# Optimization experiments

Measured on AMD Instinct MI355X. Metric: run time of the kernel, lower is better.

The kernel has to match this reference:

```python
import jax, jax.numpy as jnp
import numpy as np

N = 100000   # nodes
E = 1600000  # edges
F_IN = 64
HID = 64
N_HLIN = 64
N_PRED = 1
G = 128      # graphs in batch


def setup_inputs() -> dict:
    key = jax.random.key(0)
    ks = jax.random.split(key, 12)
    x = jax.random.normal(ks[0], (N, F_IN), dtype=jnp.float32)
    edge_index = jax.random.randint(ks[1], (2, E), 0, N, dtype=jnp.int64)
    batch = jnp.sort(jax.random.randint(ks[2], (N,), 0, G, dtype=jnp.int64))
    def glorot(k, fan_in, fan_out):
        return jax.random.normal(k, (fan_in, fan_out), dtype=jnp.float32) / np.float32(np.sqrt(fan_in))
    return {
        "x": x, "edge_index": edge_index, "batch": batch,
        "W1": glorot(ks[3], F_IN, HID), "b1": jnp.zeros((HID,), jnp.float32),
        "W2": glorot(ks[4], HID, HID),  "b2": jnp.zeros((HID,), jnp.float32),
        "W3": glorot(ks[5], HID, HID),  "b3": jnp.zeros((HID,), jnp.float32),
        "W4": glorot(ks[6], HID, N_HLIN), "b4": jnp.zeros((N_HLIN,), jnp.float32),
        "lin_w": glorot(ks[7], N_HLIN, N_PRED),
        "lin_b": jnp.zeros((N_PRED,), jnp.float32),
    }


def reference(x, edge_index, batch, W1, b1, W2, b2, W3, b3, W4, b4, lin_w, lin_b):
    # GCNConv semantics (PyG default): add self-loops, symmetric deg^-1/2 normalization,
    # h' = scatter_add(norm * (h W)[src] -> dst) + b
    loop = jnp.arange(N, dtype=edge_index.dtype)
    src = jnp.concatenate([edge_index[0], loop])  # [E+N]
    dst = jnp.concatenate([edge_index[1], loop])  # [E+N]
    deg = jax.ops.segment_sum(jnp.ones_like(dst, dtype=x.dtype), dst, num_segments=N)
    dis = deg ** -0.5  # deg >= 1 thanks to self-loops
    norm = (dis[src] * dis[dst])[:, None]  # [E+N, 1]

    def gcn_conv(h, W, b):
        h = h @ W                      # [N, out]
        msg = h[src] * norm            # edge gather + scale
        agg = jax.ops.segment_sum(msg, dst, num_segments=N)  # scatter-add
        return agg + b

    h = jax.nn.relu(gcn_conv(x, W1, b1))
    h = jax.nn.relu(gcn_conv(h, W2, b2))
    h = jax.nn.relu(gcn_conv(h, W3, b3))
    h = gcn_conv(h, W4, b4)

    # global_mean_pool over graph ids
    sums = jax.ops.segment_sum(h, batch, num_segments=G)          # [G, N_HLIN]
    cnts = jax.ops.segment_sum(jnp.ones((N,), h.dtype), batch, num_segments=G)
    pooled = sums / jnp.maximum(cnts, 1.0)[:, None]
    # dropout is identity in eval mode
    return pooled @ lin_w + lin_b  # [G, N_PRED]
```

## Files before the change

### kernel.cpp

```cpp
#include <hip/hip_runtime.h>
#include <type_traits>

#define NN 100000
#define NE 1600000
#define FD 64
#define NG 128
#define NB ((NN + 255) >> 8)
#define CAP 6144
#define SRCMASK 0x1FFFF
#define ZR NN

typedef _Float16 f16x8 __attribute__((ext_vector_type(8)));
typedef _Float16 f16x4 __attribute__((ext_vector_type(4)));
typedef float f32x4 __attribute__((ext_vector_type(4)));

__global__ void bhist_k(const int* __restrict__ dst, int* __restrict__ bhist) {
    __shared__ int h[NB];
    int t = threadIdx.x;
    for (int i = t; i < NB; i += 256) h[i] = 0;
    __syncthreads();
    int base = blockIdx.x * 4096;
#pragma unroll
    for (int i = 0; i < 16; i++) {
        int e = base + i * 256 + t;
        if (e < NE) atomicAdd(&h[dst[e] >> 8], 1);
    }
    __syncthreads();
    for (int i = t; i < NB; i += 256)
        if (h[i]) atomicAdd(&bhist[i], h[i]);
}

__global__ void bscan_k(const int* __restrict__ bhist, int* __restrict__ bbase,
                        int* __restrict__ gcursor, _Float16* __restrict__ zrow) {
    __shared__ int sS[512];
    int t = threadIdx.x;
    if (t < 8) ((int4*)zrow)[t] = make_int4(0, 0, 0, 0);
    sS[t] = (t < NB) ? bhist[t] : 0;
    __syncthreads();
    for (int off = 1; off < 512; off <<= 1) {
        int x = (t >= off) ? sS[t - off] : 0;
        __syncthreads();
        if (t >= off) sS[t] += x;
        __syncthreads();
    }
    int excl = (t == 0) ? 0 : sS[t - 1];
    if (t < NB) { bbase[t] = excl; gcursor[t] = excl; }
    if (t == NB) bbase[NB] = NE;
}

__global__ void part1_k(const int* __restrict__ src, const int* __restrict__ dst,
                        int* __restrict__ gcursor, int* __restrict__ part) {
    __shared__ int hist[NB];
    __shared__ int resv[NB];
    __shared__ int lcur[NB];
    int t = threadIdx.x;
    for (int i = t; i < NB; i += 256) { hist[i] = 0; lcur[i] = 0; }
    __syncthreads();
    int base = blockIdx.x * 4096;
    int s[16], d[16];
#pragma unroll
    for (int i = 0; i < 16; i++) {
        int e = base + i * 256 + t;
        if (e < NE) {
            s[i] = src[e]; d[i] = dst[e];
            atomicAdd(&hist[d[i] >> 8], 1);
        } else d[i] = -1;
    }
    __syncthreads();
    for (int b = t; b < NB; b += 256)
        if (hist[b]) resv[b] = atomicAdd(&gcursor[b], hist[b]);
    __syncthreads();
#pragma unroll
    for (int i = 0; i < 16; i++) {
        if (d[i] >= 0) {
            int b = d[i] >> 8;
            int off = atomicAdd(&lcur[b], 1);
            part[resv[b] + off] = s[i] | ((d[i] & 255) << 17);
        }
    }
}

__global__ void csr2_k(const int* __restrict__ part, const int* __restrict__ bbase,
                       int* __restrict__ rowptr, float* __restrict__ dis,
                       int* __restrict__ entries) {
    __shared__ int sA[CAP];
    __shared__ int sB[CAP];
    __shared__ int cntL[256];
    __shared__ int posL[256];
    __shared__ int locL[256];
    int b = blockIdx.x, t = threadIdx.x;
    int n0 = b << 8;
    int nCnt = min(256, NN - n0);
    cntL[t] = 0; posL[t] = 0;
    __syncthreads();
    int e0 = bbase[b], e1 = bbase[b + 1];
    int cnt = e1 - e0;

    for (int i = t; i < cnt; i += 256) {
        int pk = part[e0 + i];
        if (i < CAP) sA[i] = pk;
        atomicAdd(&cntL[(pk >> 17) & 255], 1);
    }
    __syncthreads();

    locL[t] = cntL[t];
    __syncthreads();
    for (int off = 1; off < 256; off <<= 1) {
        int x = (t >= off) ? locL[t - off] : 0;
        __syncthreads();
        if (t >= off) locL[t] += x;
        __syncthreads();
    }
    int excl = (t == 0) ? 0 : locL[t - 1];
    __syncthreads();
    locL[t] = excl;
    __syncthreads();

    if (t < nCnt) {
        rowptr[n0 + t] = e0 + locL[t];
        dis[n0 + t] = rsqrtf((float)cntL[t] + 1.0f);
    }
    if (b == NB - 1 && t == 0) rowptr[NN] = NE;

    for (int i = t; i < cnt; i += 256) {
        int pk = (i < CAP) ? sA[i] : part[e0 + i];
        int ln = (pk >> 17) & 255;
        int sv = pk & SRCMASK;
        int pos = atomicAdd(&posL[ln], 1);
        int idx = locL[ln] + pos;
        if (idx < CAP) sB[idx] = sv;
        else entries[e0 + idx] = sv;
    }
    __syncthreads();
    int lim = min(cnt, CAP);
    for (int i = t; i < lim; i += 256)
        entries[e0 + i] = sB[i];
}

template <typename TIN>
__global__ __launch_bounds__(256) void gemm_mfma_k(const TIN* __restrict__ h,
                                                   const float* __restrict__ W,
                                                   const float* __restrict__ dis,
                                                   _Float16* __restrict__ out16) {
    __shared__ _Float16 wT[64 * 76];
    __shared__ _Float16 oS[64 * 64];
    int t = threadIdx.x;
    int wave = t >> 6, lane = t & 63;
    int m0 = blockIdx.x * 64 + wave * 16;
    int arow = min(m0 + (lane & 15), NN - 1);
    int kg = lane >> 4;

    f16x8 a0, a1;
    if constexpr (std::is_same<TIN, float>::value) {
        const float4* p0 = (const float4*)&h[(size_t)arow * 64 + kg * 8];
        const float4* p1 = (const float4*)&h[(size_t)arow * 64 + 32 + kg * 8];
        float4 x0 = p0[0], x1 = p0[1], y0 = p1[0], y1 = p1[1];
        a0[0] = (_Float16)x0.x; a0[1] = (_Float16)x0.y; a0[2] = (_Float16)x0.z; a0[3] = (_Float16)x0.w;
        a0[4] = (_Float16)x1.x; a0[5] = (_Float16)x1.y; a0[6] = (_Float16)x1.z; a0[7] = (_Float16)x1.w;
        a1[0] = (_Float16)y0.x; a1[1] = (_Float16)y0.y; a1[2] = (_Float16)y0.z; a1[3] = (_Float16)y0.w;
        a1[4] = (_Float16)y1.x; a1[5] = (_Float16)y1.y; a1[6] = (_Float16)y1.z; a1[7] = (_Float16)y1.w;
    } else {
        a0 = *(const f16x8*)&h[(size_t)arow * 64 + kg * 8];
        a1 = *(const f16x8*)&h[(size_t)arow * 64 + 32 + kg * 8];
    }

    for (int i = t; i < 4096; i += 256) {
        int k = i >> 6, c = i & 63;
        wT[c * 76 + k] = (_Float16)W[i];
    }
    __syncthreads();

    f32x4 acc[4];
#pragma unroll
    for (int i = 0; i < 4; i++) acc[i] = (f32x4){0.f, 0.f, 0.f, 0.f};

#pragma unroll
    for (int c0 = 0; c0 < 4; c0++) {
        const _Float16* wp = &wT[(c0 * 16 + (lane & 15)) * 76 + kg * 8];
        f16x8 b0 = *(const f16x8*)wp;
        f16x8 b1 = *(const f16x8*)(wp + 32);
        acc[c0] = __builtin_amdgcn_mfma_f32_16x16x32_f16(a0, b0, acc[c0], 0, 0, 0);
        acc[c0] = __builtin_amdgcn_mfma_f32_16x16x32_f16(a1, b1, acc[c0], 0, 0, 0);
    }

#pragma unroll
    for (int j = 0; j < 4; j++) {
        int row = (lane >> 4) * 4 + j;
        float dsc = dis[min(m0 + row, NN - 1)];
#pragma unroll
        for (int c0 = 0; c0 < 4; c0++)
            oS[(wave * 16 + row) * 64 + c0 * 16 + (lane & 15)] = (_Float16)(acc[c0][j] * dsc);
    }
    __syncthreads();

    int rbase = blockIdx.x * 64;
    for (int i = t; i < 512; i += 256) {
        int r = i >> 3;
        if (rbase + r < NN)
            ((int4*)&out16[(size_t)(rbase + r) * 64])[i & 7] = ((int4*)oS)[i];
    }
}

template <int LAST>
__global__ void gather_k(const _Float16* __restrict__ h2p, const int* __restrict__ rowptr,
                         const int* __restrict__ entries, const float* __restrict__ dis,
                         const float* __restrict__ bias, _Float16* __restrict__ out16,
                         float* __restrict__ outf) {
    int wave = (blockIdx.x * blockDim.x + threadIdx.x) >> 6;
    int lane = threadIdx.x & 63;
    int g = lane >> 3;
    int k = lane & 7;
    int fo = k * 8;
    int gb = g << 3;

    int n = wave * 8 + g;
    bool valid = n < NN;
    int nc = valid ? n : NN - 1;
    int e0 = rowptr[nc];
    int cnt = valid ? (rowptr[nc + 1] - e0 + 1) : 0;

    int m = cnt;
    m = max(m, __shfl_xor(m, 8));
    m = max(m, __shfl_xor(m, 16));
    m = max(m, __shfl_xor(m, 32));
    int nch = (m + 7) >> 3;

    float ac[8];
#pragma unroll
    for (int i = 0; i < 8; i++) ac[i] = 0.f;

    int itk = k;
    int entA = (itk == 0) ? (valid ? n : ZR)
             : ((itk < cnt) ? entries[e0 + itk - 1] : ZR);

    for (int ch = 0; ch < nch; ++ch) {
        int itk2 = ((ch + 1) << 3) + k;
        int entB = (itk2 < cnt) ? entries[e0 + itk2 - 1] : ZR;
#pragma unroll
        for (int c = 0; c < 8; ++c) {
            int s = __shfl(entA, gb | c);
            f16x8 v = *(const f16x8*)&h2p[(size_t)s * 64 + fo];
#pragma unroll
            for (int i = 0; i < 8; ++i) ac[i] += (float)v[i];
        }
        entA = entB;
    }

    if (valid) {
        float dn = dis[n];
        float4 b0 = *(const float4*)&bias[fo];
        float4 b1 = *(const float4*)&bias[fo + 4];
        float r0 = b0.x + dn * ac[0], r1 = b0.y + dn * ac[1];
        float r2 = b0.z + dn * ac[2], r3 = b0.w + dn * ac[3];
        float r4 = b1.x + dn * ac[4], r5 = b1.y + dn * ac[5];
        float r6 = b1.z + dn * ac[6], r7 = b1.w + dn * ac[7];
        if (LAST) {
            *(float4*)&outf[(size_t)n * 64 + fo]     = make_float4(r0, r1, r2, r3);
            *(float4*)&outf[(size_t)n * 64 + fo + 4] = make_float4(r4, r5, r6, r7);
        } else {
            f16x8 o;
            o[0] = (_Float16)fmaxf(r0, 0.f); o[1] = (_Float16)fmaxf(r1, 0.f);
            o[2] = (_Float16)fmaxf(r2, 0.f); o[3] = (_Float16)fmaxf(r3, 0.f);
            o[4] = (_Float16)fmaxf(r4, 0.f); o[5] = (_Float16)fmaxf(r5, 0.f);
            o[6] = (_Float16)fmaxf(r6, 0.f); o[7] = (_Float16)fmaxf(r7, 0.f);
            *(f16x8*)&out16[(size_t)n * 64 + fo] = o;
        }
    }
}

__global__ void pool_acc_k(const float* __restrict__ h, const int* __restrict__ batch,
                           float* __restrict__ pool) {
    int wid = (blockIdx.x * blockDim.x + threadIdx.x) >> 6;
    int lane = threadIdx.x & 63;
    int n0 = wid * 32;
    if (n0 >= NN) return;
    int n1 = min(n0 + 32, NN);
    int g = batch[n0];
    float acc = 0.0f;
    for (int n = n0; n < n1; n++) {
        int gn = batch[n];
        if (gn != g) {
            atomicAdd(&pool[g * FD + lane], acc);
            acc = 0.0f;
            g = gn;
        }
        acc += h[(size_t)n * FD + lane];
    }
    atomicAdd(&pool[g * FD + lane], acc);
}

__global__ void cnt_k(const int* __restrict__ batch, float* __restrict__ cnt,
                      float* __restrict__ pool) {
    int t = threadIdx.x;
    for (int i = t; i < NG * FD; i += 128) pool[i] = 0.f;
    if (t >= NG) return;
    auto lb = [&](int key) {
        int lo = 0, hi = NN;
        while (lo < hi) {
            int mid = (lo + hi) >> 1;
            if (batch[mid] < key) lo = mid + 1; else hi = mid;
        }
        return lo;
    };
    cnt[t] = (float)(lb(t + 1) - lb(t));
}

__global__ void final_k(const float* __restrict__ pool, const float* __restrict__ cnt,
                        const float* __restrict__ lin_w, const float* __restrict__ lin_b,
                        float* __restrict__ out) {
    int g = blockIdx.x * blockDim.x + threadIdx.x;
    if (g >= NG) return;
    float c = fmaxf(cnt[g], 1.0f);
    float s = 0.0f;
    for (int f = 0; f < FD; f++) s += pool[g * FD + f] * lin_w[f];
    out[g] = s / c + lin_b[0];
}

extern "C" void kernel_launch(void* const* d_in, const int* in_sizes, int n_in,
                              void* d_out, int out_size, void* d_ws, size_t ws_size,
                              hipStream_t stream) {
    const float* x     = (const float*)d_in[0];
    const int*   src   = (const int*)d_in[1];
    const int*   dst   = ((const int*)d_in[1]) + NE;
    const int*   batch = (const int*)d_in[2];
    const float* W1 = (const float*)d_in[3];  const float* b1 = (const float*)d_in[4];
    const float* W2 = (const float*)d_in[5];  const float* b2 = (const float*)d_in[6];
    const float* W3 = (const float*)d_in[7];  const float* b3 = (const float*)d_in[8];
    const float* W4 = (const float*)d_in[9];  const float* b4 = (const float*)d_in[10];
    const float* lin_w = (const float*)d_in[11];
    const float* lin_b = (const float*)d_in[12];
    float* out = (float*)d_out;

    char* p = (char*)d_ws;
    float*    aggf    = (float*)p;
    int*      part    = (int*)p;      p += (size_t)NN * FD * 4;
    _Float16* h16a    = (_Float16*)p; p += (size_t)(NN + 1) * FD * 2;
    _Float16* h16b    = (_Float16*)p; p += (size_t)(NN + 1) * FD * 2;
    int*      entries = (int*)p;      p += (size_t)NE * 4;
    float*    dis     = (float*)p;    p += (size_t)NN * 4;
    int*      rowptr  = (int*)p;      p += (size_t)(NN + 4) * 4;
    int*      bhist   = (int*)p;      p += ((NB + 3) & ~3) * 4;
    int*      bbase   = (int*)p;      p += ((NB + 4) & ~3) * 4;
    int*      gcursor = (int*)p;      p += ((NB + 3) & ~3) * 4;
    float*    pool    = (float*)p;    p += (size_t)NG * FD * 4;
    float*    cnt     = (float*)p;    p += (size_t)NG * 4;

    const int EGRID = (NE + 4095) / 4096;

    hipMemsetAsync(bhist, 0, NB * 4, stream);
    bhist_k<<<EGRID, 256, 0, stream>>>(dst, bhist);
    bscan_k<<<1, 512, 0, stream>>>(bhist, bbase, gcursor, h16b + (size_t)ZR * FD);
    part1_k<<<EGRID, 256, 0, stream>>>(src, dst, gcursor, part);
    csr2_k<<<NB, 256, 0, stream>>>(part, bbase, rowptr, dis, entries);

    const int GEMM_GRID = (NN + 63) / 64;
    const int GATHER_GRID = (NN + 31) / 32;

    gemm_mfma_k<float><<<GEMM_GRID, 256, 0, stream>>>(x, W1, dis, h16b);
    gather_k<0><<<GATHER_GRID, 256, 0, stream>>>(h16b, rowptr, entries, dis, b1, h16a, nullptr);
    gemm_mfma_k<_Float16><<<GEMM_GRID, 256, 0, stream>>>(h16a, W2, dis, h16b);
    gather_k<0><<<GATHER_GRID, 256, 0, stream>>>(h16b, rowptr, entries, dis, b2, h16a, nullptr);
    gemm_mfma_k<_Float16><<<GEMM_GRID, 256, 0, stream>>>(h16a, W3, dis, h16b);
    gather_k<0><<<GATHER_GRID, 256, 0, stream>>>(h16b, rowptr, entries, dis, b3, h16a, nullptr);
    gemm_mfma_k<_Float16><<<GEMM_GRID, 256, 0, stream>>>(h16a, W4, dis, h16b);
    gather_k<1><<<GATHER_GRID, 256, 0, stream>>>(h16b, rowptr, entries, dis, b4, nullptr, aggf);

    cnt_k<<<1, 128, 0, stream>>>(batch, cnt, pool);
    pool_acc_k<<<((NN + 31) / 32 * 64 + 255) / 256, 256, 0, stream>>>(aggf, batch, pool);
    final_k<<<1, 128, 0, stream>>>(pool, cnt, lin_w, lin_b, out);
}
```

Before: 273.9 us.

## Fuse gather with next-layer GEMM and process nodes in degree-sorted order

Each GCN layer's neighbor aggregation, bias and ReLU are now fused with the next layer's dense 64x64 MFMA transform in one kernel. This removes the intermediate fp16 write and re-read between gather and GEMM for layers 2-4. A degree-bucketed permutation of nodes is built once, via histogram, scan and fill, so that the 8 nodes sharing a wave have similar degrees and less lane time is lost to the wave's max-degree loop. The cost is extra setup kernels and scattered output writes through the permutation. It also needs ping-pong zero rows in both buffers for padded neighbors.

```diff
diff --git a/kernel.cpp b/kernel.cpp
--- a/kernel.cpp
+++ b/kernel.cpp
@@ -9,9 +9,9 @@
 #define CAP 6144
 #define SRCMASK 0x1FFFF
 #define ZR NN
+#define NPAD 100032
 
 typedef _Float16 f16x8 __attribute__((ext_vector_type(8)));
-typedef _Float16 f16x4 __attribute__((ext_vector_type(4)));
 typedef float f32x4 __attribute__((ext_vector_type(4)));
 
 __global__ void bhist_k(const int* __restrict__ dst, int* __restrict__ bhist) {
@@ -31,10 +31,12 @@
 }
 
 __global__ void bscan_k(const int* __restrict__ bhist, int* __restrict__ bbase,
-                        int* __restrict__ gcursor, _Float16* __restrict__ zrow) {
+                        int* __restrict__ gcursor, _Float16* __restrict__ zrowA,
+                        _Float16* __restrict__ zrowB) {
     __shared__ int sS[512];
     int t = threadIdx.x;
-    if (t < 8) ((int4*)zrow)[t] = make_int4(0, 0, 0, 0);
+    if (t < 8)  ((int4*)zrowA)[t] = make_int4(0, 0, 0, 0);
+    if (t >= 8 && t < 16) ((int4*)zrowB)[t - 8] = make_int4(0, 0, 0, 0);
     sS[t] = (t < NB) ? bhist[t] : 0;
     __syncthreads();
     for (int off = 1; off < 512; off <<= 1) {
@@ -82,16 +84,18 @@
 
 __global__ void csr2_k(const int* __restrict__ part, const int* __restrict__ bbase,
                        int* __restrict__ rowptr, float* __restrict__ dis,
-                       int* __restrict__ entries) {
+                       int* __restrict__ entries, int* __restrict__ dbins) {
     __shared__ int sA[CAP];
     __shared__ int sB[CAP];
     __shared__ int cntL[256];
     __shared__ int posL[256];
     __shared__ int locL[256];
+    __shared__ int dbL[64];
     int b = blockIdx.x, t = threadIdx.x;
     int n0 = b << 8;
     int nCnt = min(256, NN - n0);
     cntL[t] = 0; posL[t] = 0;
+    if (t < 64) dbL[t] = 0;
     __syncthreads();
     int e0 = bbase[b], e1 = bbase[b + 1];
     int cnt = e1 - e0;
@@ -102,6 +106,8 @@
         atomicAdd(&cntL[(pk >> 17) & 255], 1);
     }
     __syncthreads();
+
+    if (t < nCnt) atomicAdd(&dbL[min(cntL[t], 63)], 1);
 
     locL[t] = cntL[t];
     __syncthreads();
@@ -121,6 +127,7 @@
         dis[n0 + t] = rsqrtf((float)cntL[t] + 1.0f);
     }
     if (b == NB - 1 && t == 0) rowptr[NN] = NE;
+    if (t < 64 && dbL[t]) atomicAdd(&dbins[t], dbL[t]);
 
     for (int i = t; i < cnt; i += 256) {
         int pk = (i < CAP) ? sA[i] : part[e0 + i];
@@ -137,8 +144,42 @@
         entries[e0 + i] = sB[i];
 }
 
-template <typename TIN>
-__global__ __launch_bounds__(256) void gemm_mfma_k(const TIN* __restrict__ h,
+__global__ void dscan_k(const int* __restrict__ dbins, int* __restrict__ dcursor,
+                        int* __restrict__ perm) {
+    int t = threadIdx.x;
+    int orig = dbins[t];
+    int v = orig;
+    for (int off = 1; off < 64; off <<= 1) {
+        int x = __shfl_up(v, off);
+        if (t >= off) v += x;
+    }
+    dcursor[t] = v - orig;
+    if (t < NPAD - NN) perm[NN + t] = -1;
+}
+
+__global__ void dfill_k(const int* __restrict__ rowptr, int* __restrict__ dcursor,
+                        int* __restrict__ perm) {
+    __shared__ int h[64], resv[64], lpos[64];
+    int t = threadIdx.x;
+    int n = blockIdx.x * 256 + t;
+    if (t < 64) { h[t] = 0; lpos[t] = 0; }
+    __syncthreads();
+    int bin = -1;
+    if (n < NN) {
+        int deg = rowptr[n + 1] - rowptr[n];
+        bin = min(deg, 63);
+        atomicAdd(&h[bin], 1);
+    }
+    __syncthreads();
+    if (t < 64 && h[t]) resv[t] = atomicAdd(&dcursor[t], h[t]);
+    __syncthreads();
+    if (n < NN) {
+        int pos = atomicAdd(&lpos[bin], 1);
+        perm[resv[bin] + pos] = n;
+    }
+}
+
+__global__ __launch_bounds__(256) void gemm_mfma_k(const float* __restrict__ h,
                                                    const float* __restrict__ W,
                                                    const float* __restrict__ dis,
                                                    _Float16* __restrict__ out16) {
@@ -151,18 +192,13 @@
     int kg = lane >> 4;
 
     f16x8 a0, a1;
-    if constexpr (std::is_same<TIN, float>::value) {
-        const float4* p0 = (const float4*)&h[(size_t)arow * 64 + kg * 8];
-        const float4* p1 = (const float4*)&h[(size_t)arow * 64 + 32 + kg * 8];
-        float4 x0 = p0[0], x1 = p0[1], y0 = p1[0], y1 = p1[1];
-        a0[0] = (_Float16)x0.x; a0[1] = (_Float16)x0.y; a0[2] = (_Float16)x0.z; a0[3] = (_Float16)x0.w;
-        a0[4] = (_Float16)x1.x; a0[5] = (_Float16)x1.y; a0[6] = (_Float16)x1.z; a0[7] = (_Float16)x1.w;
-        a1[0] = (_Float16)y0.x; a1[1] = (_Float16)y0.y; a1[2] = (_Float16)y0.z; a1[3] = (_Float16)y0.w;
-        a1[4] = (_Float16)y1.x; a1[5] = (_Float16)y1.y; a1[6] = (_Float16)y1.z; a1[7] = (_Float16)y1.w;
-    } else {
-        a0 = *(const f16x8*)&h[(size_t)arow * 64 + kg * 8];
-        a1 = *(const f16x8*)&h[(size_t)arow * 64 + 32 + kg * 8];
-    }
+    const float4* p0 = (const float4*)&h[(size_t)arow * 64 + kg * 8];
+    const float4* p1 = (const float4*)&h[(size_t)arow * 64 + 32 + kg * 8];
+    float4 x0 = p0[0], x1 = p0[1], y0 = p1[0], y1 = p1[1];
+    a0[0] = (_Float16)x0.x; a0[1] = (_Float16)x0.y; a0[2] = (_Float16)x0.z; a0[3] = (_Float16)x0.w;
+    a0[4] = (_Float16)x1.x; a0[5] = (_Float16)x1.y; a0[6] = (_Float16)x1.z; a0[7] = (_Float16)x1.w;
+    a1[0] = (_Float16)y0.x; a1[1] = (_Float16)y0.y; a1[2] = (_Float16)y0.z; a1[3] = (_Float16)y0.w;
+    a1[4] = (_Float16)y1.x; a1[5] = (_Float16)y1.y; a1[6] = (_Float16)y1.z; a1[7] = (_Float16)y1.w;
 
     for (int i = t; i < 4096; i += 256) {
         int k = i >> 6, c = i & 63;
@@ -201,21 +237,32 @@
     }
 }
 
-template <int LAST>
-__global__ void gather_k(const _Float16* __restrict__ h2p, const int* __restrict__ rowptr,
-                         const int* __restrict__ entries, const float* __restrict__ dis,
-                         const float* __restrict__ bias, _Float16* __restrict__ out16,
-                         float* __restrict__ outf) {
-    int wave = (blockIdx.x * blockDim.x + threadIdx.x) >> 6;
-    int lane = threadIdx.x & 63;
-    int g = lane >> 3;
-    int k = lane & 7;
-    int fo = k * 8;
-    int gb = g << 3;
-
-    int n = wave * 8 + g;
-    bool valid = n < NN;
-    int nc = valid ? n : NN - 1;
+__global__ __launch_bounds__(512) void fused_k(const _Float16* __restrict__ hin,
+                                               const int* __restrict__ rowptr,
+                                               const int* __restrict__ entries,
+                                               const float* __restrict__ dis,
+                                               const float* __restrict__ bias,
+                                               const float* __restrict__ W,
+                                               const int* __restrict__ perm,
+                                               _Float16* __restrict__ hout) {
+    __shared__ _Float16 wT[64 * 76];
+    __shared__ _Float16 hT[64 * 72];
+    __shared__ _Float16 oS[64 * 64];
+    __shared__ int   permL[64];
+    __shared__ float disL[64];
+
+    int t = threadIdx.x;
+    for (int i = t; i < 4096; i += 512)
+        wT[(i & 63) * 76 + (i >> 6)] = (_Float16)W[i];
+    if (t < 64) permL[t] = perm[blockIdx.x * 64 + t];
+    __syncthreads();
+
+    int wave = t >> 6, lane = t & 63;
+    int g = lane >> 3, k = lane & 7, fo = k * 8, gb = g << 3;
+    int local = wave * 8 + g;
+    int n = permL[local];
+    bool valid = n >= 0;
+    int nc = valid ? n : 0;
     int e0 = rowptr[nc];
     int cnt = valid ? (rowptr[nc + 1] - e0 + 1) : 0;
 
@@ -229,9 +276,95 @@
 #pragma unroll
     for (int i = 0; i < 8; i++) ac[i] = 0.f;
 
-    int itk = k;
-    int entA = (itk == 0) ? (valid ? n : ZR)
-             : ((itk < cnt) ? entries[e0 + itk - 1] : ZR);
+    int entA = (k == 0) ? (valid ? n : ZR)
+             : ((k < cnt) ? entries[e0 + k - 1] : ZR);
+
+    for (int ch = 0; ch < nch; ++ch) {
+        int itk2 = ((ch + 1) << 3) + k;
+        int entB = (itk2 < cnt) ? entries[e0 + itk2 - 1] : ZR;
+#pragma unroll
+        for (int c = 0; c < 8; ++c) {
+            int s = __shfl(entA, gb | c);
+            f16x8 v = *(const f16x8*)&hin[(size_t)s * 64 + fo];
+#pragma unroll
+            for (int i = 0; i < 8; ++i) ac[i] += (float)v[i];
+        }
+        entA = entB;
+    }
+
+    float dn = valid ? dis[n] : 0.f;
+    if (k == 0) disL[local] = dn;
+    {
+        float4 b0 = *(const float4*)&bias[fo];
+        float4 b1 = *(const float4*)&bias[fo + 4];
+        f16x8 o;
+        o[0] = (_Float16)fmaxf(b0.x + dn * ac[0], 0.f);
+        o[1] = (_Float16)fmaxf(b0.y + dn * ac[1], 0.f);
+        o[2] = (_Float16)fmaxf(b0.z + dn * ac[2], 0.f);
+        o[3] = (_Float16)fmaxf(b0.w + dn * ac[3], 0.f);
+        o[4] = (_Float16)fmaxf(b1.x + dn * ac[4], 0.f);
+        o[5] = (_Float16)fmaxf(b1.y + dn * ac[5], 0.f);
+        o[6] = (_Float16)fmaxf(b1.z + dn * ac[6], 0.f);
+        o[7] = (_Float16)fmaxf(b1.w + dn * ac[7], 0.f);
+        *(f16x8*)&hT[local * 72 + fo] = o;
+    }
+    __syncthreads();
+
+#pragma unroll
+    for (int i2 = 0; i2 < 2; i2++) {
+        int tile = wave * 2 + i2;
+        int rt = tile >> 2, ct = tile & 3;
+        int arow = rt * 16 + (lane & 15);
+        int kg = lane >> 4;
+        f16x8 a0 = *(const f16x8*)&hT[arow * 72 + kg * 8];
+        f16x8 a1 = *(const f16x8*)&hT[arow * 72 + 32 + kg * 8];
+        const _Float16* wp = &wT[(ct * 16 + (lane & 15)) * 76 + kg * 8];
+        f16x8 b0 = *(const f16x8*)wp;
+        f16x8 b1 = *(const f16x8*)(wp + 32);
+        f32x4 acc = (f32x4){0.f, 0.f, 0.f, 0.f};
+        acc = __builtin_amdgcn_mfma_f32_16x16x32_f16(a0, b0, acc, 0, 0, 0);
+        acc = __builtin_amdgcn_mfma_f32_16x16x32_f16(a1, b1, acc, 0, 0, 0);
+#pragma unroll
+        for (int j = 0; j < 4; j++) {
+            int row = rt * 16 + (lane >> 4) * 4 + j;
+            oS[row * 64 + ct * 16 + (lane & 15)] = (_Float16)(acc[j] * disL[row]);
+        }
+    }
+    __syncthreads();
+
+    int r = t >> 3;
+    int nOut = permL[r];
+    if (nOut >= 0)
+        ((int4*)&hout[(size_t)nOut * 64])[t & 7] = ((int4*)oS)[t];
+}
+
+__global__ void gatherL_k(const _Float16* __restrict__ h2p, const int* __restrict__ rowptr,
+                          const int* __restrict__ entries, const float* __restrict__ dis,
+                          const float* __restrict__ bias, const int* __restrict__ perm,
+                          float* __restrict__ outf) {
+    int wave = (blockIdx.x * blockDim.x + threadIdx.x) >> 6;
+    int lane = threadIdx.x & 63;
+    int g = lane >> 3, k = lane & 7, fo = k * 8, gb = g << 3;
+
+    int idx = wave * 8 + g;
+    int n = (idx < NPAD) ? perm[idx] : -1;
+    bool valid = n >= 0;
+    int nc = valid ? n : 0;
+    int e0 = rowptr[nc];
+    int cnt = valid ? (rowptr[nc + 1] - e0 + 1) : 0;
+
+    int m = cnt;
+    m = max(m, __shfl_xor(m, 8));
+    m = max(m, __shfl_xor(m, 16));
+    m = max(m, __shfl_xor(m, 32));
+    int nch = (m + 7) >> 3;
+
+    float ac[8];
+#pragma unroll
+    for (int i = 0; i < 8; i++) ac[i] = 0.f;
+
+    int entA = (k == 0) ? (valid ? n : ZR)
+             : ((k < cnt) ? entries[e0 + k - 1] : ZR);
 
     for (int ch = 0; ch < nch; ++ch) {
         int itk2 = ((ch + 1) << 3) + k;
@@ -250,21 +383,12 @@
         float dn = dis[n];
         float4 b0 = *(const float4*)&bias[fo];
         float4 b1 = *(const float4*)&bias[fo + 4];
-        float r0 = b0.x + dn * ac[0], r1 = b0.y + dn * ac[1];
-        float r2 = b0.z + dn * ac[2], r3 = b0.w + dn * ac[3];
-        float r4 = b1.x + dn * ac[4], r5 = b1.y + dn * ac[5];
-        float r6 = b1.z + dn * ac[6], r7 = b1.w + dn * ac[7];
-        if (LAST) {
-            *(float4*)&outf[(size_t)n * 64 + fo]     = make_float4(r0, r1, r2, r3);
-            *(float4*)&outf[(size_t)n * 64 + fo + 4] = make_float4(r4, r5, r6, r7);
-        } else {
-            f16x8 o;
-            o[0] = (_Float16)fmaxf(r0, 0.f); o[1] = (_Float16)fmaxf(r1, 0.f);
-            o[2] = (_Float16)fmaxf(r2, 0.f); o[3] = (_Float16)fmaxf(r3, 0.f);
-            o[4] = (_Float16)fmaxf(r4, 0.f); o[5] = (_Float16)fmaxf(r5, 0.f);
-            o[6] = (_Float16)fmaxf(r6, 0.f); o[7] = (_Float16)fmaxf(r7, 0.f);
-            *(f16x8*)&out16[(size_t)n * 64 + fo] = o;
-        }
+        *(float4*)&outf[(size_t)n * 64 + fo] =
+            make_float4(b0.x + dn * ac[0], b0.y + dn * ac[1],
+                        b0.z + dn * ac[2], b0.w + dn * ac[3]);
+        *(float4*)&outf[(size_t)n * 64 + fo + 4] =
+            make_float4(b1.x + dn * ac[4], b1.y + dn * ac[5],
+                        b1.z + dn * ac[6], b1.w + dn * ac[7]);
     }
 }
 
@@ -340,30 +464,33 @@
     float*    dis     = (float*)p;    p += (size_t)NN * 4;
     int*      rowptr  = (int*)p;      p += (size_t)(NN + 4) * 4;
     int*      bhist   = (int*)p;      p += ((NB + 3) & ~3) * 4;
+    int*      dbins   = (int*)p;      p += 64 * 4;
     int*      bbase   = (int*)p;      p += ((NB + 4) & ~3) * 4;
     int*      gcursor = (int*)p;      p += ((NB + 3) & ~3) * 4;
+    int*      dcursor = (int*)p;      p += 64 * 4;
+    int*      perm    = (int*)p;      p += (size_t)NPAD * 4;
     float*    pool    = (float*)p;    p += (size_t)NG * FD * 4;
     float*    cnt     = (float*)p;    p += (size_t)NG * 4;
 
     const int EGRID = (NE + 4095) / 4096;
 
-    hipMemsetAsync(bhist, 0, NB * 4, stream);
+    hipMemsetAsync(bhist, 0, (((NB + 3) & ~3) + 64) * 4, stream);
     bhist_k<<<EGRID, 256, 0, stream>>>(dst, bhist);
-    bscan_k<<<1, 512, 0, stream>>>(bhist, bbase, gcursor, h16b + (size_t)ZR * FD);
+    bscan_k<<<1, 512, 0, stream>>>(bhist, bbase, gcursor,
+                                   h16a + (size_t)ZR * FD, h16b + (size_t)ZR * FD);
     part1_k<<<EGRID, 256, 0, stream>>>(src, dst, gcursor, part);
-    csr2_k<<<NB, 256, 0, stream>>>(part, bbase, rowptr, dis, entries);
-
-    const int GEMM_GRID = (NN + 63) / 64;
-    const int GATHER_GRID = (NN + 31) / 32;
-
-    gemm_mfma_k<float><<<GEMM_GRID, 256, 0, stream>>>(x, W1, dis, h16b);
-    gather_k<0><<<GATHER_GRID, 256, 0, stream>>>(h16b, rowptr, entries, dis, b1, h16a, nullptr);
-    gemm_mfma_k<_Float16><<<GEMM_GRID, 256, 0, stream>>>(h16a, W2, dis, h16b);
-    gather_k<0><<<GATHER_GRID, 256, 0, stream>>>(h16b, rowptr, entries, dis, b2, h16a, nullptr);
-    gemm_mfma_k<_Float16><<<GEMM_GRID, 256, 0, stream>>>(h16a, W3, dis, h16b);
-    gather_k<0><<<GATHER_GRID, 256, 0, stream>>>(h16b, rowptr, entries, dis, b3, h16a, nullptr);
-    gemm_mfma_k<_Float16><<<GEMM_GRID, 256, 0, stream>>>(h16a, W4, dis, h16b);
-    gather_k<1><<<GATHER_GRID, 256, 0, stream>>>(h16b, rowptr, entries, dis, b4, nullptr, aggf);
+    csr2_k<<<NB, 256, 0, stream>>>(part, bbase, rowptr, dis, entries, dbins);
+    dscan_k<<<1, 64, 0, stream>>>(dbins, dcursor, perm);
+    dfill_k<<<NB, 256, 0, stream>>>(rowptr, dcursor, perm);
+
+    const int FUSED_GRID = NPAD / 64;
+    const int GL_GRID = NPAD / 32;
+
+    gemm_mfma_k<<<(NN + 63) / 64, 256, 0, stream>>>(x, W1, dis, h16b);
+    fused_k<<<FUSED_GRID, 512, 0, stream>>>(h16b, rowptr, entries, dis, b1, W2, perm, h16a);
+    fused_k<<<FUSED_GRID, 512, 0, stream>>>(h16a, rowptr, entries, dis, b2, W3, perm, h16b);
+    fused_k<<<FUSED_GRID, 512, 0, stream>>>(h16b, rowptr, entries, dis, b3, W4, perm, h16a);
+    gatherL_k<<<GL_GRID, 256, 0, stream>>>(h16a, rowptr, entries, dis, b4, perm, aggf);
 
     cnt_k<<<1, 128, 0, stream>>>(batch, cnt, pool);
     pool_acc_k<<<((NN + 31) / 32 * 64 + 255) / 256, 256, 0, stream>>>(aggf, batch, pool);
```

Result: no change. 269.3 us (-1.7%).

## Sort nodes by degree so gather waves process similar-length rows

Applied to the files above, without the earlier changes.

Builds a degree histogram in csr2_k, scans it, and fills a permutation array that groups nodes by in-degree (capped at 63). The gather kernels then map each 8-lane group to a node from this permutation, so the eight nodes in a wave have near-equal neighbor counts and the wave runs fewer idle chunks. This adds two small kernels and an extra indirection, and it scatters output writes and self-row reads, losing the locality of consecutive node order. Padding entries are marked -1 and the zero row is now written in both feature buffers.

```diff
diff --git a/kernel.cpp b/kernel.cpp
--- a/kernel.cpp
+++ b/kernel.cpp
@@ -9,9 +9,9 @@
 #define CAP 6144
 #define SRCMASK 0x1FFFF
 #define ZR NN
+#define NPAD 100032
 
 typedef _Float16 f16x8 __attribute__((ext_vector_type(8)));
-typedef _Float16 f16x4 __attribute__((ext_vector_type(4)));
 typedef float f32x4 __attribute__((ext_vector_type(4)));
 
 __global__ void bhist_k(const int* __restrict__ dst, int* __restrict__ bhist) {
@@ -31,10 +31,12 @@
 }
 
 __global__ void bscan_k(const int* __restrict__ bhist, int* __restrict__ bbase,
-                        int* __restrict__ gcursor, _Float16* __restrict__ zrow) {
+                        int* __restrict__ gcursor, _Float16* __restrict__ zrowA,
+                        _Float16* __restrict__ zrowB) {
     __shared__ int sS[512];
     int t = threadIdx.x;
-    if (t < 8) ((int4*)zrow)[t] = make_int4(0, 0, 0, 0);
+    if (t < 8)  ((int4*)zrowA)[t] = make_int4(0, 0, 0, 0);
+    if (t >= 8 && t < 16) ((int4*)zrowB)[t - 8] = make_int4(0, 0, 0, 0);
     sS[t] = (t < NB) ? bhist[t] : 0;
     __syncthreads();
     for (int off = 1; off < 512; off <<= 1) {
@@ -82,16 +84,18 @@
 
 __global__ void csr2_k(const int* __restrict__ part, const int* __restrict__ bbase,
                        int* __restrict__ rowptr, float* __restrict__ dis,
-                       int* __restrict__ entries) {
+                       int* __restrict__ entries, int* __restrict__ dbins) {
     __shared__ int sA[CAP];
     __shared__ int sB[CAP];
     __shared__ int cntL[256];
     __shared__ int posL[256];
     __shared__ int locL[256];
+    __shared__ int dbL[64];
     int b = blockIdx.x, t = threadIdx.x;
     int n0 = b << 8;
     int nCnt = min(256, NN - n0);
     cntL[t] = 0; posL[t] = 0;
+    if (t < 64) dbL[t] = 0;
     __syncthreads();
     int e0 = bbase[b], e1 = bbase[b + 1];
     int cnt = e1 - e0;
@@ -102,6 +106,8 @@
         atomicAdd(&cntL[(pk >> 17) & 255], 1);
     }
     __syncthreads();
+
+    if (t < nCnt) atomicAdd(&dbL[min(cntL[t], 63)], 1);
 
     locL[t] = cntL[t];
     __syncthreads();
@@ -121,6 +127,7 @@
         dis[n0 + t] = rsqrtf((float)cntL[t] + 1.0f);
     }
     if (b == NB - 1 && t == 0) rowptr[NN] = NE;
+    if (t < 64 && dbL[t]) atomicAdd(&dbins[t], dbL[t]);
 
     for (int i = t; i < cnt; i += 256) {
         int pk = (i < CAP) ? sA[i] : part[e0 + i];
@@ -135,6 +142,41 @@
     int lim = min(cnt, CAP);
     for (int i = t; i < lim; i += 256)
         entries[e0 + i] = sB[i];
+}
+
+__global__ void dscan_k(const int* __restrict__ dbins, int* __restrict__ dcursor,
+                        int* __restrict__ perm) {
+    int t = threadIdx.x;
+    int orig = dbins[t];
+    int v = orig;
+    for (int off = 1; off < 64; off <<= 1) {
+        int x = __shfl_up(v, off);
+        if (t >= off) v += x;
+    }
+    dcursor[t] = v - orig;
+    if (t < NPAD - NN) perm[NN + t] = -1;
+}
+
+__global__ void dfill_k(const int* __restrict__ rowptr, int* __restrict__ dcursor,
+                        int* __restrict__ perm) {
+    __shared__ int h[64], resv[64], lpos[64];
+    int t = threadIdx.x;
+    int n = blockIdx.x * 256 + t;
+    if (t < 64) { h[t] = 0; lpos[t] = 0; }
+    __syncthreads();
+    int bin = -1;
+    if (n < NN) {
+        int deg = rowptr[n + 1] - rowptr[n];
+        bin = min(deg, 63);
+        atomicAdd(&h[bin], 1);
+    }
+    __syncthreads();
+    if (t < 64 && h[t]) resv[t] = atomicAdd(&dcursor[t], h[t]);
+    __syncthreads();
+    if (n < NN) {
+        int pos = atomicAdd(&lpos[bin], 1);
+        perm[resv[bin] + pos] = n;
+    }
 }
 
 template <typename TIN>
@@ -204,8 +246,8 @@
 template <int LAST>
 __global__ void gather_k(const _Float16* __restrict__ h2p, const int* __restrict__ rowptr,
                          const int* __restrict__ entries, const float* __restrict__ dis,
-                         const float* __restrict__ bias, _Float16* __restrict__ out16,
-                         float* __restrict__ outf) {
+                         const float* __restrict__ bias, const int* __restrict__ perm,
+                         _Float16* __restrict__ out16, float* __restrict__ outf) {
     int wave = (blockIdx.x * blockDim.x + threadIdx.x) >> 6;
     int lane = threadIdx.x & 63;
     int g = lane >> 3;
@@ -213,9 +255,9 @@
     int fo = k * 8;
     int gb = g << 3;
 
-    int n = wave * 8 + g;
-    bool valid = n < NN;
-    int nc = valid ? n : NN - 1;
+    int n = perm[wave * 8 + g];
+    bool valid = n >= 0;
+    int nc = valid ? n : 0;
     int e0 = rowptr[nc];
     int cnt = valid ? (rowptr[nc + 1] - e0 + 1) : 0;
 
@@ -229,9 +271,8 @@
 #pragma unroll
     for (int i = 0; i < 8; i++) ac[i] = 0.f;
 
-    int itk = k;
-    int entA = (itk == 0) ? (valid ? n : ZR)
-             : ((itk < cnt) ? entries[e0 + itk - 1] : ZR);
+    int entA = (k == 0) ? (valid ? n : ZR)
+             : ((k < cnt) ? entries[e0 + k - 1] : ZR);
 
     for (int ch = 0; ch < nch; ++ch) {
         int itk2 = ((ch + 1) << 3) + k;
@@ -340,30 +381,36 @@
     float*    dis     = (float*)p;    p += (size_t)NN * 4;
     int*      rowptr  = (int*)p;      p += (size_t)(NN + 4) * 4;
     int*      bhist   = (int*)p;      p += ((NB + 3) & ~3) * 4;
+    int*      dbins   = (int*)p;      p += 64 * 4;
     int*      bbase   = (int*)p;      p += ((NB + 4) & ~3) * 4;
     int*      gcursor = (int*)p;      p += ((NB + 3) & ~3) * 4;
+    int*      dcursor = (int*)p;      p += 64 * 4;
+    int*      perm    = (int*)p;      p += (size_t)NPAD * 4;
     float*    pool    = (float*)p;    p += (size_t)NG * FD * 4;
     float*    cnt     = (float*)p;    p += (size_t)NG * 4;
 
     const int EGRID = (NE + 4095) / 4096;
 
-    hipMemsetAsync(bhist, 0, NB * 4, stream);
+    hipMemsetAsync(bhist, 0, (((NB + 3) & ~3) + 64) * 4, stream);
     bhist_k<<<EGRID, 256, 0, stream>>>(dst, bhist);
-    bscan_k<<<1, 512, 0, stream>>>(bhist, bbase, gcursor, h16b + (size_t)ZR * FD);
+    bscan_k<<<1, 512, 0, stream>>>(bhist, bbase, gcursor,
+                                   h16a + (size_t)ZR * FD, h16b + (size_t)ZR * FD);
     part1_k<<<EGRID, 256, 0, stream>>>(src, dst, gcursor, part);
-    csr2_k<<<NB, 256, 0, stream>>>(part, bbase, rowptr, dis, entries);
+    csr2_k<<<NB, 256, 0, stream>>>(part, bbase, rowptr, dis, entries, dbins);
+    dscan_k<<<1, 64, 0, stream>>>(dbins, dcursor, perm);
+    dfill_k<<<NB, 256, 0, stream>>>(rowptr, dcursor, perm);
 
     const int GEMM_GRID = (NN + 63) / 64;
-    const int GATHER_GRID = (NN + 31) / 32;
+    const int GATHER_GRID = NPAD / 32;
 
     gemm_mfma_k<float><<<GEMM_GRID, 256, 0, stream>>>(x, W1, dis, h16b);
-    gather_k<0><<<GATHER_GRID, 256, 0, stream>>>(h16b, rowptr, entries, dis, b1, h16a, nullptr);
+    gather_k<0><<<GATHER_GRID, 256, 0, stream>>>(h16b, rowptr, entries, dis, b1, perm, h16a, nullptr);
     gemm_mfma_k<_Float16><<<GEMM_GRID, 256, 0, stream>>>(h16a, W2, dis, h16b);
-    gather_k<0><<<GATHER_GRID, 256, 0, stream>>>(h16b, rowptr, entries, dis, b2, h16a, nullptr);
+    gather_k<0><<<GATHER_GRID, 256, 0, stream>>>(h16b, rowptr, entries, dis, b2, perm, h16a, nullptr);
     gemm_mfma_k<_Float16><<<GEMM_GRID, 256, 0, stream>>>(h16a, W3, dis, h16b);
-    gather_k<0><<<GATHER_GRID, 256, 0, stream>>>(h16b, rowptr, entries, dis, b3, h16a, nullptr);
+    gather_k<0><<<GATHER_GRID, 256, 0, stream>>>(h16b, rowptr, entries, dis, b3, perm, h16a, nullptr);
     gemm_mfma_k<_Float16><<<GEMM_GRID, 256, 0, stream>>>(h16a, W4, dis, h16b);
-    gather_k<1><<<GATHER_GRID, 256, 0, stream>>>(h16b, rowptr, entries, dis, b4, nullptr, aggf);
+    gather_k<1><<<GATHER_GRID, 256, 0, stream>>>(h16b, rowptr, entries, dis, b4, perm, nullptr, aggf);
 
     cnt_k<<<1, 128, 0, stream>>>(batch, cnt, pool);
     pool_acc_k<<<((NN + 31) / 32 * 64 + 255) / 256, 256, 0, stream>>>(aggf, batch, pool);
```

Measured after the change: 290.2 us. +6.0%, slower.

## Drop bucket histogram pass using fixed-stride bucket slots and packed rowptr/degree

Applied to the files above, without the earlier changes.

Removes the separate destination-bucket histogram and scan kernels by giving each 256-node bucket a fixed slot region of BSTRIDE entries, so partitioning can start from zeroed cursors. Row pointer and degree are packed into one int, so the gather reads a single word per node. Zero-row setup, pool clearing and graph counts move into one init kernel, cutting the memset and several launches. The risks are that a bucket with more than BSTRIDE edges overflows its slot, and that degrees above 255 are clamped, which breaks correctness for high-degree nodes.

```diff
diff --git a/kernel.cpp b/kernel.cpp
--- a/kernel.cpp
+++ b/kernel.cpp
@@ -6,46 +6,33 @@
 #define FD 64
 #define NG 128
 #define NB ((NN + 255) >> 8)
+#define BSTRIDE 5120
 #define CAP 6144
 #define SRCMASK 0x1FFFF
 #define ZR NN
 
 typedef _Float16 f16x8 __attribute__((ext_vector_type(8)));
-typedef _Float16 f16x4 __attribute__((ext_vector_type(4)));
 typedef float f32x4 __attribute__((ext_vector_type(4)));
 
-__global__ void bhist_k(const int* __restrict__ dst, int* __restrict__ bhist) {
-    __shared__ int h[NB];
+__global__ void init_k(const int* __restrict__ batch, float* __restrict__ cnt,
+                       float* __restrict__ pool, int* __restrict__ gcursor,
+                       _Float16* __restrict__ zrowA, _Float16* __restrict__ zrowB) {
     int t = threadIdx.x;
-    for (int i = t; i < NB; i += 256) h[i] = 0;
-    __syncthreads();
-    int base = blockIdx.x * 4096;
-#pragma unroll
-    for (int i = 0; i < 16; i++) {
-        int e = base + i * 256 + t;
-        if (e < NE) atomicAdd(&h[dst[e] >> 8], 1);
-    }
-    __syncthreads();
-    for (int i = t; i < NB; i += 256)
-        if (h[i]) atomicAdd(&bhist[i], h[i]);
-}
-
-__global__ void bscan_k(const int* __restrict__ bhist, int* __restrict__ bbase,
-                        int* __restrict__ gcursor, _Float16* __restrict__ zrow) {
-    __shared__ int sS[512];
-    int t = threadIdx.x;
-    if (t < 8) ((int4*)zrow)[t] = make_int4(0, 0, 0, 0);
-    sS[t] = (t < NB) ? bhist[t] : 0;
-    __syncthreads();
-    for (int off = 1; off < 512; off <<= 1) {
-        int x = (t >= off) ? sS[t - off] : 0;
-        __syncthreads();
-        if (t >= off) sS[t] += x;
-        __syncthreads();
-    }
-    int excl = (t == 0) ? 0 : sS[t - 1];
-    if (t < NB) { bbase[t] = excl; gcursor[t] = excl; }
-    if (t == NB) bbase[NB] = NE;
+    if (t < 8)  ((int4*)zrowA)[t] = make_int4(0, 0, 0, 0);
+    if (t >= 8 && t < 16) ((int4*)zrowB)[t - 8] = make_int4(0, 0, 0, 0);
+    for (int i = t; i < NB; i += 512) gcursor[i] = 0;
+    for (int i = t; i < NG * FD; i += 512) pool[i] = 0.f;
+    if (t < NG) {
+        auto lb = [&](int key) {
+            int lo = 0, hi = NN;
+            while (lo < hi) {
+                int mid = (lo + hi) >> 1;
+                if (batch[mid] < key) lo = mid + 1; else hi = mid;
+            }
+            return lo;
+        };
+        cnt[t] = (float)(lb(t + 1) - lb(t));
+    }
 }
 
 __global__ void part1_k(const int* __restrict__ src, const int* __restrict__ dst,
@@ -75,13 +62,13 @@
         if (d[i] >= 0) {
             int b = d[i] >> 8;
             int off = atomicAdd(&lcur[b], 1);
-            part[resv[b] + off] = s[i] | ((d[i] & 255) << 17);
+            part[b * BSTRIDE + resv[b] + off] = s[i] | ((d[i] & 255) << 17);
         }
     }
 }
 
-__global__ void csr2_k(const int* __restrict__ part, const int* __restrict__ bbase,
-                       int* __restrict__ rowptr, float* __restrict__ dis,
+__global__ void csr2_k(const int* __restrict__ part, const int* __restrict__ gcursor,
+                       int* __restrict__ rowptrdeg, float* __restrict__ dis,
                        int* __restrict__ entries) {
     __shared__ int sA[CAP];
     __shared__ int sB[CAP];
@@ -93,8 +80,8 @@
     int nCnt = min(256, NN - n0);
     cntL[t] = 0; posL[t] = 0;
     __syncthreads();
-    int e0 = bbase[b], e1 = bbase[b + 1];
-    int cnt = e1 - e0;
+    int e0 = b * BSTRIDE;
+    int cnt = gcursor[b];
 
     for (int i = t; i < cnt; i += 256) {
         int pk = part[e0 + i];
@@ -117,10 +104,9 @@
     __syncthreads();
 
     if (t < nCnt) {
-        rowptr[n0 + t] = e0 + locL[t];
+        rowptrdeg[n0 + t] = ((e0 + locL[t]) << 8) | min(cntL[t], 255);
         dis[n0 + t] = rsqrtf((float)cntL[t] + 1.0f);
     }
-    if (b == NB - 1 && t == 0) rowptr[NN] = NE;
 
     for (int i = t; i < cnt; i += 256) {
         int pk = (i < CAP) ? sA[i] : part[e0 + i];
@@ -202,7 +188,7 @@
 }
 
 template <int LAST>
-__global__ void gather_k(const _Float16* __restrict__ h2p, const int* __restrict__ rowptr,
+__global__ void gather_k(const _Float16* __restrict__ h2p, const int* __restrict__ rowptrdeg,
                          const int* __restrict__ entries, const float* __restrict__ dis,
                          const float* __restrict__ bias, _Float16* __restrict__ out16,
                          float* __restrict__ outf) {
@@ -215,9 +201,9 @@
 
     int n = wave * 8 + g;
     bool valid = n < NN;
-    int nc = valid ? n : NN - 1;
-    int e0 = rowptr[nc];
-    int cnt = valid ? (rowptr[nc + 1] - e0 + 1) : 0;
+    int rp = rowptrdeg[valid ? n : NN - 1];
+    int e0 = rp >> 8;
+    int cnt = valid ? (rp & 255) + 1 : 0;
 
     int m = cnt;
     m = max(m, __shfl_xor(m, 8));
@@ -229,9 +215,8 @@
 #pragma unroll
     for (int i = 0; i < 8; i++) ac[i] = 0.f;
 
-    int itk = k;
-    int entA = (itk == 0) ? (valid ? n : ZR)
-             : ((itk < cnt) ? entries[e0 + itk - 1] : ZR);
+    int entA = (k == 0) ? (valid ? n : ZR)
+             : ((k < cnt) ? entries[e0 + k - 1] : ZR);
 
     for (int ch = 0; ch < nch; ++ch) {
         int itk2 = ((ch + 1) << 3) + k;
@@ -289,22 +274,6 @@
     atomicAdd(&pool[g * FD + lane], acc);
 }
 
-__global__ void cnt_k(const int* __restrict__ batch, float* __restrict__ cnt,
-                      float* __restrict__ pool) {
-    int t = threadIdx.x;
-    for (int i = t; i < NG * FD; i += 128) pool[i] = 0.f;
-    if (t >= NG) return;
-    auto lb = [&](int key) {
-        int lo = 0, hi = NN;
-        while (lo < hi) {
-            int mid = (lo + hi) >> 1;
-            if (batch[mid] < key) lo = mid + 1; else hi = mid;
-        }
-        return lo;
-    };
-    cnt[t] = (float)(lb(t + 1) - lb(t));
-}
-
 __global__ void final_k(const float* __restrict__ pool, const float* __restrict__ cnt,
                         const float* __restrict__ lin_w, const float* __restrict__ lin_b,
                         float* __restrict__ out) {
@@ -332,40 +301,36 @@
     float* out = (float*)d_out;
 
     char* p = (char*)d_ws;
-    float*    aggf    = (float*)p;
-    int*      part    = (int*)p;      p += (size_t)NN * FD * 4;
-    _Float16* h16a    = (_Float16*)p; p += (size_t)(NN + 1) * FD * 2;
-    _Float16* h16b    = (_Float16*)p; p += (size_t)(NN + 1) * FD * 2;
-    int*      entries = (int*)p;      p += (size_t)NE * 4;
-    float*    dis     = (float*)p;    p += (size_t)NN * 4;
-    int*      rowptr  = (int*)p;      p += (size_t)(NN + 4) * 4;
-    int*      bhist   = (int*)p;      p += ((NB + 3) & ~3) * 4;
-    int*      bbase   = (int*)p;      p += ((NB + 4) & ~3) * 4;
-    int*      gcursor = (int*)p;      p += ((NB + 3) & ~3) * 4;
-    float*    pool    = (float*)p;    p += (size_t)NG * FD * 4;
-    float*    cnt     = (float*)p;    p += (size_t)NG * 4;
+    float*    aggf     = (float*)p;
+    int*      part     = (int*)p;      p += (size_t)NN * FD * 4;
+    _Float16* h16a     = (_Float16*)p; p += (size_t)(NN + 1) * FD * 2;
+    _Float16* h16b     = (_Float16*)p; p += (size_t)(NN + 1) * FD * 2;
+    int*      entries  = (int*)p;      p += (size_t)NB * BSTRIDE * 4;
+    float*    dis      = (float*)p;    p += (size_t)NN * 4;
+    int*      rowptrdeg= (int*)p;      p += (size_t)((NN + 3) & ~3) * 4;
+    int*      gcursor  = (int*)p;      p += ((NB + 3) & ~3) * 4;
+    float*    pool     = (float*)p;    p += (size_t)NG * FD * 4;
+    float*    cnt      = (float*)p;    p += (size_t)NG * 4;
 
     const int EGRID = (NE + 4095) / 4096;
 
-    hipMemsetAsync(bhist, 0, NB * 4, stream);
-    bhist_k<<<EGRID, 256, 0, stream>>>(dst, bhist);
-    bscan_k<<<1, 512, 0, stream>>>(bhist, bbase, gcursor, h16b + (size_t)ZR * FD);
+    init_k<<<1, 512, 0, stream>>>(batch, cnt, pool, gcursor,
+                                  h16a + (size_t)ZR * FD, h16b + (size_t)ZR * FD);
     part1_k<<<EGRID, 256, 0, stream>>>(src, dst, gcursor, part);
-    csr2_k<<<NB, 256, 0, stream>>>(part, bbase, rowptr, dis, entries);
+    csr2_k<<<NB, 256, 0, stream>>>(part, gcursor, rowptrdeg, dis, entries);
 
     const int GEMM_GRID = (NN + 63) / 64;
     const int GATHER_GRID = (NN + 31) / 32;
 
     gemm_mfma_k<float><<<GEMM_GRID, 256, 0, stream>>>(x, W1, dis, h16b);
-    gather_k<0><<<GATHER_GRID, 256, 0, stream>>>(h16b, rowptr, entries, dis, b1, h16a, nullptr);
+    gather_k<0><<<GATHER_GRID, 256, 0, stream>>>(h16b, rowptrdeg, entries, dis, b1, h16a, nullptr);
     gemm_mfma_k<_Float16><<<GEMM_GRID, 256, 0, stream>>>(h16a, W2, dis, h16b);
-    gather_k<0><<<GATHER_GRID, 256, 0, stream>>>(h16b, rowptr, entries, dis, b2, h16a, nullptr);
+    gather_k<0><<<GATHER_GRID, 256, 0, stream>>>(h16b, rowptrdeg, entries, dis, b2, h16a, nullptr);
     gemm_mfma_k<_Float16><<<GEMM_GRID, 256, 0, stream>>>(h16a, W3, dis, h16b);
-    gather_k<0><<<GATHER_GRID, 256, 0, stream>>>(h16b, rowptr, entries, dis, b3, h16a, nullptr);
+    gather_k<0><<<GATHER_GRID, 256, 0, stream>>>(h16b, rowptrdeg, entries, dis, b3, h16a, nullptr);
     gemm_mfma_k<_Float16><<<GEMM_GRID, 256, 0, stream>>>(h16a, W4, dis, h16b);
-    gather_k<1><<<GATHER_GRID, 256, 0, stream>>>(h16b, rowptr, entries, dis, b4, nullptr, aggf);
-
-    cnt_k<<<1, 128, 0, stream>>>(batch, cnt, pool);
+    gather_k<1><<<GATHER_GRID, 256, 0, stream>>>(h16b, rowptrdeg, entries, dis, b4, nullptr, aggf);
+
     pool_acc_k<<<((NN + 31) / 32 * 64 + 255) / 256, 256, 0, stream>>>(aggf, batch, pool);
     final_k<<<1, 128, 0, stream>>>(pool, cnt, lin_w, lin_b, out);
 }
```

Measured after the change: 245.8 us. 10.3% less time.
